# Optimization experiments

Measured on AMD Instinct MI355X. Metric: run time of the kernel, lower is better.

The kernel has to match this reference:

```python
import jax, jax.numpy as jnp
import numpy as np

N_NODES = 50000
N_EDGES = 800000
H = 64      # node_hidden_size
S = 16      # static_feature_size
EF = 16     # edge_feature_size
ATT_IN = 2 * H + 2 * S + EF   # 176
ATT_W = 2 * H + EF            # 144
UPD_IN = 2 * H                # 128
UPD_W = 2 * H                 # 128


def setup_inputs() -> dict:
    key = jax.random.key(0)
    ks = jax.random.split(key, 12)
    x = jax.random.normal(ks[0], (N_NODES, H), dtype=jnp.float32)
    x_s = jax.random.normal(ks[1], (N_NODES, S), dtype=jnp.float32)
    edge_index = jax.random.randint(ks[2], (2, N_EDGES), 0, N_NODES, dtype=jnp.int32)
    edge_features = jax.random.normal(ks[3], (N_EDGES, EF), dtype=jnp.float32)

    def lin(k, out_dim, in_dim):
        lim = 1.0 / np.sqrt(in_dim)
        kw, kb = jax.random.split(k)
        W = jax.random.uniform(kw, (out_dim, in_dim), minval=-lim, maxval=lim, dtype=jnp.float32)
        b = jax.random.uniform(kb, (out_dim,), minval=-lim, maxval=lim, dtype=jnp.float32)
        return W, b

    att_w1, att_b1 = lin(ks[4], ATT_W, ATT_IN)
    att_w2, att_b2 = lin(ks[5], 1, ATT_W)
    upd_w1, upd_b1 = lin(ks[6], UPD_W, UPD_IN)
    upd_w2, upd_b2 = lin(ks[7], H, UPD_W)

    return {
        "x": x, "x_s": x_s, "edge_index": edge_index, "edge_features": edge_features,
        "att_w1": att_w1, "att_b1": att_b1, "att_w2": att_w2, "att_b2": att_b2,
        "upd_w1": upd_w1, "upd_b1": upd_b1, "upd_w2": upd_w2, "upd_b2": upd_b2,
    }


def segment_softmax(scores, segment_ids, num_segments):
    max_scores = jax.ops.segment_max(scores, segment_ids, num_segments=num_segments)
    exp_scores = jnp.exp(scores - max_scores[segment_ids])
    sum_exp = jax.ops.segment_sum(exp_scores, segment_ids, num_segments=num_segments)
    return exp_scores / (sum_exp[segment_ids] + 1e-9)


def reference(x, x_s, edge_index, edge_features,
              att_w1, att_b1, att_w2, att_b2,
              upd_w1, upd_b1, upd_w2, upd_b2):
    num_nodes = x.shape[0]
    src, dst = edge_index[0], edge_index[1]

    # gather per-edge features: [E, 2H+2S+EF]
    att_in = jnp.concatenate(
        [x[src], x[dst], x_s[src], x_s[dst], edge_features], axis=-1)

    # attention MLP (depth=1, relu hidden), squeeze to [E]
    h = jax.nn.relu(att_in @ att_w1.T + att_b1)
    raw = (h @ att_w2.T + att_b2).squeeze(-1)
    raw = jax.nn.leaky_relu(raw)

    attn = segment_softmax(raw, dst, num_nodes)

    # weighted scatter-sum of source hidden feats -> [N, H]
    aggregated = jax.ops.segment_sum(x[src] * attn[:, None], dst, num_segments=num_nodes)

    upd_in = jnp.concatenate([x, aggregated], axis=-1)
    u = jax.nn.relu(upd_in @ upd_w1.T + upd_b1)
    out = u @ upd_w2.T + upd_b2
    return jax.nn.relu(out)
```

## Files before the change

### kernel.cpp

```cpp
#include <hip/hip_runtime.h>
#include <math.h>

#define N_NODES_C 50000
#define E_C       800000
#define ATT_IN_C  176
#define ATT_HID_C 144
#define SCAN_B    98
#define UPD_TILES 3125
#define DEG_B     3125
#define CVT_B     8228
#define SCORE_B   512
#define SCORE_WAVES (SCORE_B * 4)

typedef __attribute__((ext_vector_type(8))) __bf16 bf16x8;
typedef __attribute__((ext_vector_type(4))) float f32x4;

#define O_RAW   0L
#define O_DEG   3201024L
#define O_OFF   3402752L
#define O_CUR   3603456L
#define O_CSR   3804160L
#define O_EFB   16605184L
#define O_XB    42206208L
#define O_XSB   48607232L
#define O_W1B   50208256L
#define O_UW1B  50259968L
#define O_UW2B  50293760L
#define O_AGGB  50311168L
#define O_PSUM  O_AGGB

__device__ __forceinline__ bf16x8 bzero8() {
    bf16x8 z;
#pragma unroll
    for (int i = 0; i < 8; ++i) z[i] = (__bf16)0.0f;
    return z;
}

__global__ __launch_bounds__(256) void k_prep(
    const int* __restrict__ ei,
    const float* __restrict__ x, const float* __restrict__ xs,
    const float* __restrict__ ef, const float* __restrict__ w1,
    const float* __restrict__ uw1, const float* __restrict__ uw2,
    int* __restrict__ deg,
    __bf16* __restrict__ xb, __bf16* __restrict__ xsb,
    __bf16* __restrict__ efb, __bf16* __restrict__ w1b,
    __bf16* __restrict__ uw1b, __bf16* __restrict__ uw2b)
{
    int bid = blockIdx.x;
    if (bid < DEG_B) {
        int e = bid * 256 + threadIdx.x;
        if (e < E_C) atomicAdd(&deg[ei[E_C + e]], 1);
        return;
    }
    long g = (long)(bid - DEG_B) * 256 + threadIdx.x;
    const long G_X = 400000, G_XS = 500000, G_EF = 2100000,
               G_W1 = 2103168, G_UW1 = 2105216, G_UW2 = 2106240;
    if (g >= G_UW2) return;
    const float* src; __bf16* dst; long off;
    if (g < G_X)        { src = x;   dst = xb;   off = g * 8; }
    else if (g < G_XS)  { src = xs;  dst = xsb;  off = (g - G_X) * 8; }
    else if (g < G_EF)  { src = ef;  dst = efb;  off = (g - G_XS) * 8; }
    else if (g < G_W1)  { src = w1;  dst = w1b;  off = (g - G_EF) * 8; }
    else if (g < G_UW1) { src = uw1; dst = uw1b; off = (g - G_W1) * 8; }
    else                { src = uw2; dst = uw2b; off = (g - G_UW1) * 8; }
    float4 a = *(const float4*)(src + off);
    float4 b = *(const float4*)(src + off + 4);
    bf16x8 o;
    o[0] = (__bf16)a.x; o[1] = (__bf16)a.y; o[2] = (__bf16)a.z; o[3] = (__bf16)a.w;
    o[4] = (__bf16)b.x; o[5] = (__bf16)b.y; o[6] = (__bf16)b.z; o[7] = (__bf16)b.w;
    *(bf16x8*)(dst + off) = o;
}

__global__ __launch_bounds__(256) void k_scan1(const int* __restrict__ deg,
                                               int* __restrict__ psum) {
    __shared__ int red[256];
    int b = blockIdx.x, t = threadIdx.x;
    int i = b * 512 + t * 2;
    int s = 0;
    if (i < N_NODES_C) s += deg[i];
    if (i + 1 < N_NODES_C) s += deg[i + 1];
    red[t] = s;
    __syncthreads();
#pragma unroll
    for (int off = 128; off > 0; off >>= 1) {
        if (t < off) red[t] += red[t + off];
        __syncthreads();
    }
    if (t == 0) psum[b] = red[0];
}

__global__ __launch_bounds__(256) void k_scan3(const int* __restrict__ deg,
                                               const int* __restrict__ psum,
                                               int* __restrict__ offsets,
                                               int* __restrict__ cursor) {
    __shared__ int sc[256];
    __shared__ int bo[2];
    int b = blockIdx.x, t = threadIdx.x;
    if (t < 64) {
        int v1 = (t < SCAN_B) ? psum[t] : 0;
        int v2 = (t + 64 < SCAN_B) ? psum[t + 64] : 0;
        int c   = ((t < b) ? v1 : 0) + ((t + 64 < b) ? v2 : 0);
        int tot = v1 + v2;
#pragma unroll
        for (int off = 32; off > 0; off >>= 1) {
            c   += __shfl_xor(c, off, 64);
            tot += __shfl_xor(tot, off, 64);
        }
        if (t == 0) { bo[0] = c; bo[1] = tot; }
    }
    int i = b * 512 + t * 2;
    int d0 = (i < N_NODES_C) ? deg[i] : 0;
    int d1 = (i + 1 < N_NODES_C) ? deg[i + 1] : 0;
    int s = d0 + d1;
    sc[t] = s;
    __syncthreads();
#pragma unroll
    for (int off = 1; off < 256; off <<= 1) {
        int val = sc[t];
        int add = (t >= off) ? sc[t - off] : 0;
        __syncthreads();
        sc[t] = val + add;
        __syncthreads();
    }
    int excl = bo[0] + sc[t] - s;
    if (i < N_NODES_C)     { offsets[i]     = excl;      cursor[i]     = excl; }
    if (i + 1 < N_NODES_C) { offsets[i + 1] = excl + d0; cursor[i + 1] = excl + d0; }
    if (b == 0 && t == 0)  offsets[N_NODES_C] = bo[1];
}

__global__ __launch_bounds__(256) void k_fill(const int* __restrict__ ei,
                                              int* __restrict__ cursor,
                                              int4* __restrict__ csr) {
    int e = blockIdx.x * blockDim.x + threadIdx.x;
    if (e < E_C) {
        int src  = ei[e];
        int dst  = ei[E_C + e];
        int slot = atomicAdd(&cursor[dst], 1);
        csr[slot] = make_int4(src, dst, e, 0);
    }
}

__device__ __forceinline__ void load_afrags(
    int src, int dst, int e, int quad,
    const __bf16* __restrict__ xb, const __bf16* __restrict__ xsb,
    const __bf16* __restrict__ efb,
    bf16x8 a[6])
{
    const __bf16* px = xb + (long)src * 64 + quad * 8;
    const __bf16* pd = xb + (long)dst * 64 + quad * 8;
    a[0] = *(const bf16x8*)(px);
    a[1] = *(const bf16x8*)(px + 32);
    a[2] = *(const bf16x8*)(pd);
    a[3] = *(const bf16x8*)(pd + 32);
    if (quad < 2) {
        a[4] = *(const bf16x8*)(xsb + (long)src * 16 + quad * 8);
        a[5] = *(const bf16x8*)(efb + (long)e * 16 + quad * 8);
    } else {
        a[4] = *(const bf16x8*)(xsb + (long)dst * 16 + (quad - 2) * 8);
        a[5] = bzero8();
    }
}

__global__ __launch_bounds__(256) void k_scores_mfma(
    const __bf16* __restrict__ xb, const __bf16* __restrict__ xsb,
    const __bf16* __restrict__ efb, const __bf16* __restrict__ w1b,
    const int4* __restrict__ csr,
    const float* __restrict__ b1, const float* __restrict__ w2,
    const float* __restrict__ b2, float* __restrict__ raw)
{
    __shared__ __bf16 w1s[144 * 184];
    int tid  = threadIdx.x;
    int lane = tid & 63;

    for (int c = tid; c < 144 * 22; c += 256) {
        int n = c / 22, kk = (c % 22) * 8;
        *(bf16x8*)&w1s[n * 184 + kk] = *(const bf16x8*)(w1b + (long)n * ATT_IN_C + kk);
    }
    for (int n = tid; n < 144; n += 256)
        *(bf16x8*)&w1s[n * 184 + 176] = bzero8();
    __syncthreads();

    int w = blockIdx.x * 4 + (tid >> 6);
    const int NP = E_C / 32;
    int per = (NP + SCORE_WAVES - 1) / SCORE_WAVES;
    long j0 = (long)w * per;
    long j1 = j0 + per; if (j1 > NP) j1 = NP;
    if (j0 >= j1) return;

    int mrow = lane & 15;
    int quad = lane >> 4;
    const __bf16* wls = &w1s[mrow * 184 + quad * 8];

    float b1v[9], w2v[9];
#pragma unroll
    for (int nt = 0; nt < 9; ++nt) {
        int n = nt * 16 + mrow;
        b1v[nt] = b1[n];
        w2v[nt] = w2[n];
    }
    float b2v = b2[0];

    bf16x8 curA[6], curB[6], nxtA[6], nxtB[6];
    int4 cA = make_int4(0, 0, 0, 0), cB = cA;
    {
        int4 e0 = csr[j0 * 32 + mrow];
        int4 e1 = csr[j0 * 32 + 16 + mrow];
        load_afrags(e0.x, e0.y, e0.z, quad, xb, xsb, efb, curA);
        load_afrags(e1.x, e1.y, e1.z, quad, xb, xsb, efb, curB);
        if (j0 + 1 < j1) {
            int4 f0 = csr[(j0 + 1) * 32 + mrow];
            int4 f1 = csr[(j0 + 1) * 32 + 16 + mrow];
            load_afrags(f0.x, f0.y, f0.z, quad, xb, xsb, efb, nxtA);
            load_afrags(f1.x, f1.y, f1.z, quad, xb, xsb, efb, nxtB);
        }
    }

    for (long j = j0; j < j1; ++j) {
        if (j + 2 < j1) {
            cA = csr[(j + 2) * 32 + mrow];
            cB = csr[(j + 2) * 32 + 16 + mrow];
        }

        f32x4 accA[9], accB[9];
#pragma unroll
        for (int nt = 0; nt < 9; ++nt) {
            accA[nt] = (f32x4){0.f, 0.f, 0.f, 0.f};
            accB[nt] = (f32x4){0.f, 0.f, 0.f, 0.f};
        }

#pragma unroll
        for (int ks = 0; ks < 6; ++ks) {
#pragma unroll
            for (int nt = 0; nt < 9; ++nt) {
                bf16x8 bf = *(const bf16x8*)(wls + nt * (16 * 184) + ks * 32);
                accA[nt] = __builtin_amdgcn_mfma_f32_16x16x32_bf16(
                    curA[ks], bf, accA[nt], 0, 0, 0);
                accB[nt] = __builtin_amdgcn_mfma_f32_16x16x32_bf16(
                    curB[ks], bf, accB[nt], 0, 0, 0);
            }
        }

        float pA0 = 0.f, pA1 = 0.f, pA2 = 0.f, pA3 = 0.f;
        float pB0 = 0.f, pB1 = 0.f, pB2 = 0.f, pB3 = 0.f;
#pragma unroll
        for (int nt = 0; nt < 9; ++nt) {
            pA0 += w2v[nt] * fmaxf(accA[nt][0] + b1v[nt], 0.f);
            pA1 += w2v[nt] * fmaxf(accA[nt][1] + b1v[nt], 0.f);
            pA2 += w2v[nt] * fmaxf(accA[nt][2] + b1v[nt], 0.f);
            pA3 += w2v[nt] * fmaxf(accA[nt][3] + b1v[nt], 0.f);
            pB0 += w2v[nt] * fmaxf(accB[nt][0] + b1v[nt], 0.f);
            pB1 += w2v[nt] * fmaxf(accB[nt][1] + b1v[nt], 0.f);
            pB2 += w2v[nt] * fmaxf(accB[nt][2] + b1v[nt], 0.f);
            pB3 += w2v[nt] * fmaxf(accB[nt][3] + b1v[nt], 0.f);
        }
#pragma unroll
        for (int off = 1; off < 16; off <<= 1) {
            pA0 += __shfl_xor(pA0, off, 64);
            pA1 += __shfl_xor(pA1, off, 64);
            pA2 += __shfl_xor(pA2, off, 64);
            pA3 += __shfl_xor(pA3, off, 64);
            pB0 += __shfl_xor(pB0, off, 64);
            pB1 += __shfl_xor(pB1, off, 64);
            pB2 += __shfl_xor(pB2, off, 64);
            pB3 += __shfl_xor(pB3, off, 64);
        }
        if (mrow < 4) {
            float vA = (mrow == 0) ? pA0 : (mrow == 1) ? pA1 : (mrow == 2) ? pA2 : pA3;
            float vB = (mrow == 0) ? pB0 : (mrow == 1) ? pB1 : (mrow == 2) ? pB2 : pB3;
            vA += b2v; vB += b2v;
            vA = (vA >= 0.f) ? vA : 0.01f * vA;
            vB = (vB >= 0.f) ? vB : 0.01f * vB;
            raw[(j * 2) * 16 + quad * 4 + mrow]     = vA;
            raw[(j * 2 + 1) * 16 + quad * 4 + mrow] = vB;
        }

#pragma unroll
        for (int i = 0; i < 6; ++i) { curA[i] = nxtA[i]; curB[i] = nxtB[i]; }
        if (j + 2 < j1) {
            load_afrags(cA.x, cA.y, cA.z, quad, xb, xsb, efb, nxtA);
            load_afrags(cB.x, cB.y, cB.z, quad, xb, xsb, efb, nxtB);
        }
    }
}

__global__ __launch_bounds__(256) void k_agg(
    const __bf16* __restrict__ xb, const int* __restrict__ offsets,
    const int4* __restrict__ csr,
    const float* __restrict__ raw, __bf16* __restrict__ aggb)
{
    int tid = threadIdx.x;
    int wave = tid >> 6, lane = tid & 63;
    int v = blockIdx.x * 4 + wave;
    if (v >= N_NODES_C) return;
    int s0 = offsets[v], s1 = offsets[v + 1];

    float m = -INFINITY;
    for (int p = s0 + lane; p < s1; p += 64) m = fmaxf(m, raw[p]);
#pragma unroll
    for (int off = 32; off > 0; off >>= 1) m = fmaxf(m, __shfl_xor(m, off, 64));

    float acc = 0.f, sum = 0.f;
    int p = s0;
    for (; p + 4 <= s1; p += 4) {
        int4 c0 = csr[p], c1 = csr[p + 1], c2 = csr[p + 2], c3 = csr[p + 3];
        float r0 = raw[p], r1 = raw[p + 1], r2 = raw[p + 2], r3 = raw[p + 3];
        float v0 = (float)xb[(long)c0.x * 64 + lane];
        float v1 = (float)xb[(long)c1.x * 64 + lane];
        float v2 = (float)xb[(long)c2.x * 64 + lane];
        float v3 = (float)xb[(long)c3.x * 64 + lane];
        float w0 = expf(r0 - m), w1 = expf(r1 - m);
        float w2 = expf(r2 - m), w3 = expf(r3 - m);
        sum += (w0 + w1) + (w2 + w3);
        acc += w0 * v0 + w1 * v1 + w2 * v2 + w3 * v3;
    }
    for (; p < s1; ++p) {
        int src = csr[p].x;
        float w = expf(raw[p] - m);
        sum += w;
        acc += w * (float)xb[(long)src * 64 + lane];
    }
    aggb[(long)v * 64 + lane] = (__bf16)(acc / (sum + 1e-9f));
}

__global__ __launch_bounds__(256) void k_upd_mfma(
    const __bf16* __restrict__ xb, const __bf16* __restrict__ aggb,
    const __bf16* __restrict__ w1b, const float* __restrict__ b1,
    const __bf16* __restrict__ w2b, const float* __restrict__ b2,
    float* __restrict__ out)
{
    __shared__ __bf16 ubuf[4][16 * 136];
    int tid = threadIdx.x, wid = tid >> 6, lane = tid & 63;
    int tile = blockIdx.x * 4 + wid;
    if (tile >= UPD_TILES) return;
    int mrow = lane & 15, quad = lane >> 4;

    long node = (long)tile * 16 + mrow;
    bf16x8 a1[4];
    a1[0] = *(const bf16x8*)(xb + node * 64 + quad * 8);
    a1[1] = *(const bf16x8*)(xb + node * 64 + 32 + quad * 8);
    a1[2] = *(const bf16x8*)(aggb + node * 64 + quad * 8);
    a1[3] = *(const bf16x8*)(aggb + node * 64 + 32 + quad * 8);

    bf16x8 b1f[4][8];
#pragma unroll
    for (int ks = 0; ks < 4; ++ks)
#pragma unroll
        for (int nt = 0; nt < 8; ++nt)
            b1f[ks][nt] = *(const bf16x8*)(w1b + (long)(nt * 16 + mrow) * 128 + ks * 32 + quad * 8);

    f32x4 acc1[8];
#pragma unroll
    for (int nt = 0; nt < 8; ++nt) acc1[nt] = (f32x4){0.f, 0.f, 0.f, 0.f};
#pragma unroll
    for (int ks = 0; ks < 4; ++ks)
#pragma unroll
        for (int nt = 0; nt < 8; ++nt)
            acc1[nt] = __builtin_amdgcn_mfma_f32_16x16x32_bf16(a1[ks], b1f[ks][nt], acc1[nt], 0, 0, 0);

    __bf16* ub = ubuf[wid];
#pragma unroll
    for (int nt = 0; nt < 8; ++nt) {
        float bb = b1[nt * 16 + mrow];
#pragma unroll
        for (int r = 0; r < 4; ++r) {
            float h = fmaxf(acc1[nt][r] + bb, 0.f);
            ub[(quad * 4 + r) * 136 + nt * 16 + mrow] = (__bf16)h;
        }
    }

    bf16x8 a2[4];
#pragma unroll
    for (int ks = 0; ks < 4; ++ks)
        a2[ks] = *(bf16x8*)&ub[mrow * 136 + ks * 32 + quad * 8];

    bf16x8 b2f[4][4];
#pragma unroll
    for (int ks = 0; ks < 4; ++ks)
#pragma unroll
        for (int nt = 0; nt < 4; ++nt)
            b2f[ks][nt] = *(const bf16x8*)(w2b + (long)(nt * 16 + mrow) * 128 + ks * 32 + quad * 8);

    f32x4 acc2[4];
#pragma unroll
    for (int nt = 0; nt < 4; ++nt) acc2[nt] = (f32x4){0.f, 0.f, 0.f, 0.f};
#pragma unroll
    for (int ks = 0; ks < 4; ++ks)
#pragma unroll
        for (int nt = 0; nt < 4; ++nt)
            acc2[nt] = __builtin_amdgcn_mfma_f32_16x16x32_bf16(a2[ks], b2f[ks][nt], acc2[nt], 0, 0, 0);

#pragma unroll
    for (int nt = 0; nt < 4; ++nt) {
        float bb = b2[nt * 16 + mrow];
#pragma unroll
        for (int r = 0; r < 4; ++r) {
            long nodeo = (long)tile * 16 + quad * 4 + r;
            out[nodeo * 64 + nt * 16 + mrow] = fmaxf(acc2[nt][r] + bb, 0.f);
        }
    }
}

extern "C" void kernel_launch(void* const* d_in, const int* in_sizes, int n_in,
                              void* d_out, int out_size, void* d_ws, size_t ws_size,
                              hipStream_t stream) {
    const float* x    = (const float*)d_in[0];
    const float* xs   = (const float*)d_in[1];
    const int*   ei   = (const int*)d_in[2];
    const float* ef   = (const float*)d_in[3];
    const float* aw1  = (const float*)d_in[4];
    const float* ab1  = (const float*)d_in[5];
    const float* aw2  = (const float*)d_in[6];
    const float* ab2  = (const float*)d_in[7];
    const float* uw1  = (const float*)d_in[8];
    const float* ub1  = (const float*)d_in[9];
    const float* uw2  = (const float*)d_in[10];
    const float* ub2  = (const float*)d_in[11];
    float* out = (float*)d_out;

    char* ws = (char*)d_ws;
    float*  raw     = (float*)(ws + O_RAW);
    int*    deg     = (int*)(ws + O_DEG);
    int*    offsets = (int*)(ws + O_OFF);
    int*    cursor  = (int*)(ws + O_CUR);
    int4*   csr     = (int4*)(ws + O_CSR);
    __bf16* efb     = (__bf16*)(ws + O_EFB);
    __bf16* xb      = (__bf16*)(ws + O_XB);
    __bf16* xsb     = (__bf16*)(ws + O_XSB);
    __bf16* w1b     = (__bf16*)(ws + O_W1B);
    __bf16* uw1b    = (__bf16*)(ws + O_UW1B);
    __bf16* uw2b    = (__bf16*)(ws + O_UW2B);
    __bf16* aggb    = (__bf16*)(ws + O_AGGB);
    int*    psum    = (int*)(ws + O_PSUM);

    hipMemsetAsync(deg, 0, N_NODES_C * sizeof(int), stream);
    hipLaunchKernelGGL(k_prep,     dim3(DEG_B + CVT_B),           dim3(256), 0, stream,
                       ei, x, xs, ef, aw1, uw1, uw2, deg, xb, xsb, efb, w1b, uw1b, uw2b);
    hipLaunchKernelGGL(k_scan1,    dim3(SCAN_B),                  dim3(256), 0, stream, deg, psum);
    hipLaunchKernelGGL(k_scan3,    dim3(SCAN_B),                  dim3(256), 0, stream,
                       deg, psum, offsets, cursor);
    hipLaunchKernelGGL(k_fill,     dim3((E_C + 255) / 256),       dim3(256), 0, stream,
                       ei, cursor, csr);
    hipLaunchKernelGGL(k_scores_mfma, dim3(SCORE_B),              dim3(256), 0, stream,
                       xb, xsb, efb, w1b, csr, ab1, aw2, ab2, raw);
    hipLaunchKernelGGL(k_agg,      dim3((N_NODES_C + 3) / 4),     dim3(256), 0, stream,
                       xb, offsets, csr, raw, aggb);
    hipLaunchKernelGGL(k_upd_mfma, dim3((UPD_TILES + 3) / 4),     dim3(256), 0, stream,
                       xb, aggb, uw1b, ub1, uw2b, ub2, out);
}
```

Before: 374.0 us.

## Precompute per-node destination projection and pack CSR entries into 32 bits

Splits the attention first-layer matmul so the destination-node terms (x[dst], x_s[dst]) plus bias are computed once per node in a new kernel and stored as fp16. The per-edge MFMA loop then covers only source and edge features, halving its K depth, and gathers the precomputed destination partials. CSR entries are packed as 16-bit src and dst in one word, and edge features are converted to bf16 in CSR order inside the fill kernel. The packing assumes node ids fit in 16 bits, but N_NODES is 50000 and fits. The fp16 partial sums and the extra gathers add some rounding error and memory traffic.

```diff
diff --git a/kernel.cpp b/kernel.cpp
--- a/kernel.cpp
+++ b/kernel.cpp
@@ -8,26 +8,29 @@
 #define SCAN_B    98
 #define UPD_TILES 3125
 #define DEG_B     3125
-#define CVT_B     8228
+#define CVT_B     1978
 #define SCORE_B   512
 #define SCORE_WAVES (SCORE_B * 4)
 
 typedef __attribute__((ext_vector_type(8))) __bf16 bf16x8;
+typedef __attribute__((ext_vector_type(8))) _Float16 h16x8;
 typedef __attribute__((ext_vector_type(4))) float f32x4;
 
 #define O_RAW   0L
-#define O_DEG   3201024L
-#define O_OFF   3402752L
-#define O_CUR   3603456L
-#define O_CSR   3804160L
-#define O_EFB   16605184L
-#define O_XB    42206208L
-#define O_XSB   48607232L
-#define O_W1B   50208256L
-#define O_UW1B  50259968L
-#define O_UW2B  50293760L
-#define O_AGGB  50311168L
-#define O_PSUM  O_AGGB
+#define O_DEG   3200000L
+#define O_OFF   3400704L
+#define O_CUR   3601408L
+#define O_CSR   3802112L
+#define O_EFC   7002112L
+#define O_XB    32602112L
+#define O_XSB   39002112L
+#define O_W1B   40602112L
+#define O_UW1B  40653312L
+#define O_UW2B  40686080L
+#define O_P8    40702464L
+#define O_P1    53502464L
+#define O_PSUM  O_P8
+#define O_AGGB  O_P8
 
 __device__ __forceinline__ bf16x8 bzero8() {
     bf16x8 z;
@@ -39,11 +42,11 @@
 __global__ __launch_bounds__(256) void k_prep(
     const int* __restrict__ ei,
     const float* __restrict__ x, const float* __restrict__ xs,
-    const float* __restrict__ ef, const float* __restrict__ w1,
+    const float* __restrict__ w1,
     const float* __restrict__ uw1, const float* __restrict__ uw2,
     int* __restrict__ deg,
     __bf16* __restrict__ xb, __bf16* __restrict__ xsb,
-    __bf16* __restrict__ efb, __bf16* __restrict__ w1b,
+    __bf16* __restrict__ w1b,
     __bf16* __restrict__ uw1b, __bf16* __restrict__ uw2b)
 {
     int bid = blockIdx.x;
@@ -53,14 +56,13 @@
         return;
     }
     long g = (long)(bid - DEG_B) * 256 + threadIdx.x;
-    const long G_X = 400000, G_XS = 500000, G_EF = 2100000,
-               G_W1 = 2103168, G_UW1 = 2105216, G_UW2 = 2106240;
+    const long G_X = 400000, G_XS = 500000, G_W1 = 503168,
+               G_UW1 = 505216, G_UW2 = 506240;
     if (g >= G_UW2) return;
     const float* src; __bf16* dst; long off;
     if (g < G_X)        { src = x;   dst = xb;   off = g * 8; }
     else if (g < G_XS)  { src = xs;  dst = xsb;  off = (g - G_X) * 8; }
-    else if (g < G_EF)  { src = ef;  dst = efb;  off = (g - G_XS) * 8; }
-    else if (g < G_W1)  { src = w1;  dst = w1b;  off = (g - G_EF) * 8; }
+    else if (g < G_W1)  { src = w1;  dst = w1b;  off = (g - G_XS) * 8; }
     else if (g < G_UW1) { src = uw1; dst = uw1b; off = (g - G_W1) * 8; }
     else                { src = uw2; dst = uw2b; off = (g - G_UW1) * 8; }
     float4 a = *(const float4*)(src + off);
@@ -129,55 +131,115 @@
 }
 
 __global__ __launch_bounds__(256) void k_fill(const int* __restrict__ ei,
+                                              const float* __restrict__ ef,
                                               int* __restrict__ cursor,
-                                              int4* __restrict__ csr) {
+                                              unsigned* __restrict__ csrp,
+                                              __bf16* __restrict__ efc) {
     int e = blockIdx.x * blockDim.x + threadIdx.x;
     if (e < E_C) {
         int src  = ei[e];
         int dst  = ei[E_C + e];
         int slot = atomicAdd(&cursor[dst], 1);
-        csr[slot] = make_int4(src, dst, e, 0);
-    }
-}
-
-__device__ __forceinline__ void load_afrags(
-    int src, int dst, int e, int quad,
+        csrp[slot] = (unsigned)src | ((unsigned)dst << 16);
+        const float4* efp = (const float4*)(ef + (long)e * 16);
+        float4 f0 = efp[0], f1 = efp[1], f2 = efp[2], f3 = efp[3];
+        bf16x8 o0, o1;
+        o0[0] = (__bf16)f0.x; o0[1] = (__bf16)f0.y; o0[2] = (__bf16)f0.z; o0[3] = (__bf16)f0.w;
+        o0[4] = (__bf16)f1.x; o0[5] = (__bf16)f1.y; o0[6] = (__bf16)f1.z; o0[7] = (__bf16)f1.w;
+        o1[0] = (__bf16)f2.x; o1[1] = (__bf16)f2.y; o1[2] = (__bf16)f2.z; o1[3] = (__bf16)f2.w;
+        o1[4] = (__bf16)f3.x; o1[5] = (__bf16)f3.y; o1[6] = (__bf16)f3.z; o1[7] = (__bf16)f3.w;
+        __bf16* d = efc + (long)slot * 16;
+        *(bf16x8*)d       = o0;
+        *(bf16x8*)(d + 8) = o1;
+    }
+}
+
+__global__ __launch_bounds__(256) void k_nodep(
     const __bf16* __restrict__ xb, const __bf16* __restrict__ xsb,
-    const __bf16* __restrict__ efb,
-    bf16x8 a[6])
+    const __bf16* __restrict__ w1b, const float* __restrict__ b1,
+    _Float16* __restrict__ p8, _Float16* __restrict__ p1)
+{
+    __shared__ _Float16 tbuf[4][16 * 256];
+    int tid = threadIdx.x, wid = tid >> 6, lane = tid & 63;
+    int tile = blockIdx.x * 4 + wid;
+    if (tile >= UPD_TILES) return;
+    int mrow = lane & 15, quad = lane >> 4;
+
+    long node = (long)tile * 16 + mrow;
+    bf16x8 a0 = *(const bf16x8*)(xb + node * 64 + quad * 8);
+    bf16x8 a1 = *(const bf16x8*)(xb + node * 64 + 32 + quad * 8);
+    bf16x8 a2 = (quad < 2) ? *(const bf16x8*)(xsb + node * 16 + quad * 8) : bzero8();
+
+    f32x4 acc[9];
+#pragma unroll
+    for (int nt = 0; nt < 9; ++nt) acc[nt] = (f32x4){0.f, 0.f, 0.f, 0.f};
+#pragma unroll
+    for (int nt = 0; nt < 9; ++nt) {
+        long n = nt * 16 + mrow;
+        bf16x8 b0 = *(const bf16x8*)(w1b + n * 176 + 64 + quad * 8);
+        bf16x8 bm = *(const bf16x8*)(w1b + n * 176 + 96 + quad * 8);
+        bf16x8 b2 = (quad < 2) ? *(const bf16x8*)(w1b + n * 176 + 144 + quad * 8)
+                               : bzero8();
+        acc[nt] = __builtin_amdgcn_mfma_f32_16x16x32_bf16(a0, b0, acc[nt], 0, 0, 0);
+        acc[nt] = __builtin_amdgcn_mfma_f32_16x16x32_bf16(a1, bm, acc[nt], 0, 0, 0);
+        acc[nt] = __builtin_amdgcn_mfma_f32_16x16x32_bf16(a2, b2, acc[nt], 0, 0, 0);
+    }
+
+    _Float16* tb = tbuf[wid];
+#pragma unroll
+    for (int nt = 0; nt < 9; ++nt) {
+        float bb = b1[nt * 16 + mrow];
+#pragma unroll
+        for (int r = 0; r < 4; ++r)
+            tb[(quad * 4 + r) * 256 + mrow * 16 + nt] = (_Float16)(acc[nt][r] + bb);
+    }
+    long g8 = (long)tile * 2048;
+#pragma unroll
+    for (int c = 0; c < 4; ++c) {
+        int idx = c * 64 + lane;
+        int nl = idx >> 4, mr = idx & 15;
+        *(h16x8*)(p8 + g8 + (long)idx * 8) = *(const h16x8*)(tb + nl * 256 + mr * 16);
+    }
+    long g1 = (long)tile * 256;
+#pragma unroll
+    for (int c = 0; c < 4; ++c) {
+        int idx = lane * 4 + c;
+        int nl = idx >> 4, mr = idx & 15;
+        p1[g1 + idx] = tb[nl * 256 + mr * 16 + 8];
+    }
+}
+
+__device__ __forceinline__ void load_afrags2(
+    int src, long slot, int quad,
+    const __bf16* __restrict__ xb, const __bf16* __restrict__ xsb,
+    const __bf16* __restrict__ efc,
+    bf16x8 a[3])
 {
     const __bf16* px = xb + (long)src * 64 + quad * 8;
-    const __bf16* pd = xb + (long)dst * 64 + quad * 8;
     a[0] = *(const bf16x8*)(px);
     a[1] = *(const bf16x8*)(px + 32);
-    a[2] = *(const bf16x8*)(pd);
-    a[3] = *(const bf16x8*)(pd + 32);
-    if (quad < 2) {
-        a[4] = *(const bf16x8*)(xsb + (long)src * 16 + quad * 8);
-        a[5] = *(const bf16x8*)(efb + (long)e * 16 + quad * 8);
-    } else {
-        a[4] = *(const bf16x8*)(xsb + (long)dst * 16 + (quad - 2) * 8);
-        a[5] = bzero8();
-    }
-}
-
-__global__ __launch_bounds__(256) void k_scores_mfma(
+    a[2] = (quad < 2) ? *(const bf16x8*)(xsb + (long)src * 16 + quad * 8)
+                      : *(const bf16x8*)(efc + slot * 16 + (quad - 2) * 8);
+}
+
+__global__ __launch_bounds__(256, 2) void k_scores_mfma(
     const __bf16* __restrict__ xb, const __bf16* __restrict__ xsb,
-    const __bf16* __restrict__ efb, const __bf16* __restrict__ w1b,
-    const int4* __restrict__ csr,
-    const float* __restrict__ b1, const float* __restrict__ w2,
-    const float* __restrict__ b2, float* __restrict__ raw)
+    const __bf16* __restrict__ efc, const __bf16* __restrict__ w1b,
+    const unsigned* __restrict__ csrp,
+    const _Float16* __restrict__ p8, const _Float16* __restrict__ p1,
+    const float* __restrict__ w2, const float* __restrict__ b2,
+    float* __restrict__ raw)
 {
-    __shared__ __bf16 w1s[144 * 184];
+    __shared__ __bf16 w1s[144 * 104];
     int tid  = threadIdx.x;
     int lane = tid & 63;
 
-    for (int c = tid; c < 144 * 22; c += 256) {
-        int n = c / 22, kk = (c % 22) * 8;
-        *(bf16x8*)&w1s[n * 184 + kk] = *(const bf16x8*)(w1b + (long)n * ATT_IN_C + kk);
-    }
-    for (int n = tid; n < 144; n += 256)
-        *(bf16x8*)&w1s[n * 184 + 176] = bzero8();
+    for (int c = tid; c < 144 * 12; c += 256) {
+        int n = c / 12, kk = c % 12;
+        int col = (kk < 8) ? kk * 8 : (kk < 10) ? 128 + (kk - 8) * 8
+                                                : 160 + (kk - 10) * 8;
+        *(bf16x8*)&w1s[n * 104 + kk * 8] = *(const bf16x8*)(w1b + (long)n * ATT_IN_C + col);
+    }
     __syncthreads();
 
     int w = blockIdx.x * 4 + (tid >> 6);
@@ -189,36 +251,35 @@
 
     int mrow = lane & 15;
     int quad = lane >> 4;
-    const __bf16* wls = &w1s[mrow * 184 + quad * 8];
-
-    float b1v[9], w2v[9];
-#pragma unroll
-    for (int nt = 0; nt < 9; ++nt) {
-        int n = nt * 16 + mrow;
-        b1v[nt] = b1[n];
-        w2v[nt] = w2[n];
-    }
+    const __bf16* wls = &w1s[mrow * 104 + quad * 8];
+
+    float w2v[9];
+#pragma unroll
+    for (int nt = 0; nt < 9; ++nt) w2v[nt] = w2[nt * 16 + mrow];
     float b2v = b2[0];
 
-    bf16x8 curA[6], curB[6], nxtA[6], nxtB[6];
-    int4 cA = make_int4(0, 0, 0, 0), cB = cA;
+    bf16x8 curA[3], curB[3], nxtA[3], nxtB[3];
+    int curDA = 0, curDB = 0, nxtDA = 0, nxtDB = 0;
+    unsigned cA = 0, cB = 0;
     {
-        int4 e0 = csr[j0 * 32 + mrow];
-        int4 e1 = csr[j0 * 32 + 16 + mrow];
-        load_afrags(e0.x, e0.y, e0.z, quad, xb, xsb, efb, curA);
-        load_afrags(e1.x, e1.y, e1.z, quad, xb, xsb, efb, curB);
+        unsigned e0 = csrp[j0 * 32 + mrow];
+        unsigned e1 = csrp[j0 * 32 + 16 + mrow];
+        curDA = (int)(e0 >> 16); curDB = (int)(e1 >> 16);
+        load_afrags2((int)(e0 & 0xFFFFu), j0 * 32 + mrow,      quad, xb, xsb, efc, curA);
+        load_afrags2((int)(e1 & 0xFFFFu), j0 * 32 + 16 + mrow, quad, xb, xsb, efc, curB);
         if (j0 + 1 < j1) {
-            int4 f0 = csr[(j0 + 1) * 32 + mrow];
-            int4 f1 = csr[(j0 + 1) * 32 + 16 + mrow];
-            load_afrags(f0.x, f0.y, f0.z, quad, xb, xsb, efb, nxtA);
-            load_afrags(f1.x, f1.y, f1.z, quad, xb, xsb, efb, nxtB);
+            unsigned f0 = csrp[(j0 + 1) * 32 + mrow];
+            unsigned f1 = csrp[(j0 + 1) * 32 + 16 + mrow];
+            nxtDA = (int)(f0 >> 16); nxtDB = (int)(f1 >> 16);
+            load_afrags2((int)(f0 & 0xFFFFu), (j0 + 1) * 32 + mrow,      quad, xb, xsb, efc, nxtA);
+            load_afrags2((int)(f1 & 0xFFFFu), (j0 + 1) * 32 + 16 + mrow, quad, xb, xsb, efc, nxtB);
         }
     }
 
     for (long j = j0; j < j1; ++j) {
         if (j + 2 < j1) {
-            cA = csr[(j + 2) * 32 + mrow];
-            cB = csr[(j + 2) * 32 + 16 + mrow];
+            cA = csrp[(j + 2) * 32 + mrow];
+            cB = csrp[(j + 2) * 32 + 16 + mrow];
         }
 
         f32x4 accA[9], accB[9];
@@ -229,10 +290,10 @@
         }
 
 #pragma unroll
-        for (int ks = 0; ks < 6; ++ks) {
+        for (int ks = 0; ks < 3; ++ks) {
 #pragma unroll
             for (int nt = 0; nt < 9; ++nt) {
-                bf16x8 bf = *(const bf16x8*)(wls + nt * (16 * 184) + ks * 32);
+                bf16x8 bf = *(const bf16x8*)(wls + nt * (16 * 104) + ks * 32);
                 accA[nt] = __builtin_amdgcn_mfma_f32_16x16x32_bf16(
                     curA[ks], bf, accA[nt], 0, 0, 0);
                 accB[nt] = __builtin_amdgcn_mfma_f32_16x16x32_bf16(
@@ -240,19 +301,45 @@
             }
         }
 
+        int dA[4], dB[4];
+#pragma unroll
+        for (int r = 0; r < 4; ++r) {
+            int sl = (lane & 48) | (quad * 4 + r);
+            dA[r] = __shfl(curDA, sl, 64);
+            dB[r] = __shfl(curDB, sl, 64);
+        }
+        h16x8 paf[4], pbf[4];
+        float pa8[4], pb8[4];
+#pragma unroll
+        for (int r = 0; r < 4; ++r) {
+            paf[r] = *(const h16x8*)(p8 + (long)dA[r] * 128 + mrow * 8);
+            pa8[r] = (float)p1[(long)dA[r] * 16 + mrow];
+            pbf[r] = *(const h16x8*)(p8 + (long)dB[r] * 128 + mrow * 8);
+            pb8[r] = (float)p1[(long)dB[r] * 16 + mrow];
+        }
+
         float pA0 = 0.f, pA1 = 0.f, pA2 = 0.f, pA3 = 0.f;
         float pB0 = 0.f, pB1 = 0.f, pB2 = 0.f, pB3 = 0.f;
 #pragma unroll
-        for (int nt = 0; nt < 9; ++nt) {
-            pA0 += w2v[nt] * fmaxf(accA[nt][0] + b1v[nt], 0.f);
-            pA1 += w2v[nt] * fmaxf(accA[nt][1] + b1v[nt], 0.f);
-            pA2 += w2v[nt] * fmaxf(accA[nt][2] + b1v[nt], 0.f);
-            pA3 += w2v[nt] * fmaxf(accA[nt][3] + b1v[nt], 0.f);
-            pB0 += w2v[nt] * fmaxf(accB[nt][0] + b1v[nt], 0.f);
-            pB1 += w2v[nt] * fmaxf(accB[nt][1] + b1v[nt], 0.f);
-            pB2 += w2v[nt] * fmaxf(accB[nt][2] + b1v[nt], 0.f);
-            pB3 += w2v[nt] * fmaxf(accB[nt][3] + b1v[nt], 0.f);
-        }
+        for (int nt = 0; nt < 8; ++nt) {
+            pA0 += w2v[nt] * fmaxf(accA[nt][0] + (float)paf[0][nt], 0.f);
+            pA1 += w2v[nt] * fmaxf(accA[nt][1] + (float)paf[1][nt], 0.f);
+            pA2 += w2v[nt] * fmaxf(accA[nt][2] + (float)paf[2][nt], 0.f);
+            pA3 += w2v[nt] * fmaxf(accA[nt][3] + (float)paf[3][nt], 0.f);
+            pB0 += w2v[nt] * fmaxf(accB[nt][0] + (float)pbf[0][nt], 0.f);
+            pB1 += w2v[nt] * fmaxf(accB[nt][1] + (float)pbf[1][nt], 0.f);
+            pB2 += w2v[nt] * fmaxf(accB[nt][2] + (float)pbf[2][nt], 0.f);
+            pB3 += w2v[nt] * fmaxf(accB[nt][3] + (float)pbf[3][nt], 0.f);
+        }
+        pA0 += w2v[8] * fmaxf(accA[8][0] + pa8[0], 0.f);
+        pA1 += w2v[8] * fmaxf(accA[8][1] + pa8[1], 0.f);
+        pA2 += w2v[8] * fmaxf(accA[8][2] + pa8[2], 0.f);
+        pA3 += w2v[8] * fmaxf(accA[8][3] + pa8[3], 0.f);
+        pB0 += w2v[8] * fmaxf(accB[8][0] + pb8[0], 0.f);
+        pB1 += w2v[8] * fmaxf(accB[8][1] + pb8[1], 0.f);
+        pB2 += w2v[8] * fmaxf(accB[8][2] + pb8[2], 0.f);
+        pB3 += w2v[8] * fmaxf(accB[8][3] + pb8[3], 0.f);
+
 #pragma unroll
         for (int off = 1; off < 16; off <<= 1) {
             pA0 += __shfl_xor(pA0, off, 64);
@@ -275,17 +362,19 @@
         }
 
 #pragma unroll
-        for (int i = 0; i < 6; ++i) { curA[i] = nxtA[i]; curB[i] = nxtB[i]; }
+        for (int i = 0; i < 3; ++i) { curA[i] = nxtA[i]; curB[i] = nxtB[i]; }
+        curDA = nxtDA; curDB = nxtDB;
         if (j + 2 < j1) {
-            load_afrags(cA.x, cA.y, cA.z, quad, xb, xsb, efb, nxtA);
-            load_afrags(cB.x, cB.y, cB.z, quad, xb, xsb, efb, nxtB);
+            nxtDA = (int)(cA >> 16); nxtDB = (int)(cB >> 16);
+            load_afrags2((int)(cA & 0xFFFFu), (j + 2) * 32 + mrow,      quad, xb, xsb, efc, nxtA);
+            load_afrags2((int)(cB & 0xFFFFu), (j + 2) * 32 + 16 + mrow, quad, xb, xsb, efc, nxtB);
         }
     }
 }
 
 __global__ __launch_bounds__(256) void k_agg(
     const __bf16* __restrict__ xb, const int* __restrict__ offsets,
-    const int4* __restrict__ csr,
+    const unsigned* __restrict__ csrp,
     const float* __restrict__ raw, __bf16* __restrict__ aggb)
 {
     int tid = threadIdx.x;
@@ -302,19 +391,19 @@
     float acc = 0.f, sum = 0.f;
     int p = s0;
     for (; p + 4 <= s1; p += 4) {
-        int4 c0 = csr[p], c1 = csr[p + 1], c2 = csr[p + 2], c3 = csr[p + 3];
+        unsigned c0 = csrp[p], c1 = csrp[p + 1], c2 = csrp[p + 2], c3 = csrp[p + 3];
         float r0 = raw[p], r1 = raw[p + 1], r2 = raw[p + 2], r3 = raw[p + 3];
-        float v0 = (float)xb[(long)c0.x * 64 + lane];
-        float v1 = (float)xb[(long)c1.x * 64 + lane];
-        float v2 = (float)xb[(long)c2.x * 64 + lane];
-        float v3 = (float)xb[(long)c3.x * 64 + lane];
+        float v0 = (float)xb[(long)(c0 & 0xFFFFu) * 64 + lane];
+        float v1 = (float)xb[(long)(c1 & 0xFFFFu) * 64 + lane];
+        float v2 = (float)xb[(long)(c2 & 0xFFFFu) * 64 + lane];
+        float v3 = (float)xb[(long)(c3 & 0xFFFFu) * 64 + lane];
         float w0 = expf(r0 - m), w1 = expf(r1 - m);
         float w2 = expf(r2 - m), w3 = expf(r3 - m);
         sum += (w0 + w1) + (w2 + w3);
         acc += w0 * v0 + w1 * v1 + w2 * v2 + w3 * v3;
     }
     for (; p < s1; ++p) {
-        int src = csr[p].x;
+        int src = (int)(csrp[p] & 0xFFFFu);
         float w = expf(raw[p] - m);
         sum += w;
         acc += w * (float)xb[(long)src * 64 + lane];
@@ -418,32 +507,36 @@
     float* out = (float*)d_out;
 
     char* ws = (char*)d_ws;
-    float*  raw     = (float*)(ws + O_RAW);
-    int*    deg     = (int*)(ws + O_DEG);
-    int*    offsets = (int*)(ws + O_OFF);
-    int*    cursor  = (int*)(ws + O_CUR);
-    int4*   csr     = (int4*)(ws + O_CSR);
-    __bf16* efb     = (__bf16*)(ws + O_EFB);
-    __bf16* xb      = (__bf16*)(ws + O_XB);
-    __bf16* xsb     = (__bf16*)(ws + O_XSB);
-    __bf16* w1b     = (__bf16*)(ws + O_W1B);
-    __bf16* uw1b    = (__bf16*)(ws + O_UW1B);
-    __bf16* uw2b    = (__bf16*)(ws + O_UW2B);
-    __bf16* aggb    = (__bf16*)(ws + O_AGGB);
-    int*    psum    = (int*)(ws + O_PSUM);
+    float*     raw     = (float*)(ws + O_RAW);
+    int*       deg     = (int*)(ws + O_DEG);
+    int*       offsets = (int*)(ws + O_OFF);
+    int*       cursor  = (int*)(ws + O_CUR);
+    unsigned*  csrp    = (unsigned*)(ws + O_CSR);
+    __bf16*    efc     = (__bf16*)(ws + O_EFC);
+    __bf16*    xb      = (__bf16*)(ws + O_XB);
+    __bf16*    xsb     = (__bf16*)(ws + O_XSB);
+    __bf16*    w1b     = (__bf16*)(ws + O_W1B);
+    __bf16*    uw1b    = (__bf16*)(ws + O_UW1B);
+    __bf16*    uw2b    = (__bf16*)(ws + O_UW2B);
+    _Float16*  p8      = (_Float16*)(ws + O_P8);
+    _Float16*  p1      = (_Float16*)(ws + O_P1);
+    __bf16*    aggb    = (__bf16*)(ws + O_AGGB);
+    int*       psum    = (int*)(ws + O_PSUM);
 
     hipMemsetAsync(deg, 0, N_NODES_C * sizeof(int), stream);
     hipLaunchKernelGGL(k_prep,     dim3(DEG_B + CVT_B),           dim3(256), 0, stream,
-                       ei, x, xs, ef, aw1, uw1, uw2, deg, xb, xsb, efb, w1b, uw1b, uw2b);
+                       ei, x, xs, aw1, uw1, uw2, deg, xb, xsb, w1b, uw1b, uw2b);
     hipLaunchKernelGGL(k_scan1,    dim3(SCAN_B),                  dim3(256), 0, stream, deg, psum);
     hipLaunchKernelGGL(k_scan3,    dim3(SCAN_B),                  dim3(256), 0, stream,
                        deg, psum, offsets, cursor);
     hipLaunchKernelGGL(k_fill,     dim3((E_C + 255) / 256),       dim3(256), 0, stream,
-                       ei, cursor, csr);
+                       ei, ef, cursor, csrp, efc);
+    hipLaunchKernelGGL(k_nodep,    dim3((UPD_TILES + 3) / 4),     dim3(256), 0, stream,
+                       xb, xsb, w1b, ab1, p8, p1);
     hipLaunchKernelGGL(k_scores_mfma, dim3(SCORE_B),              dim3(256), 0, stream,
-                       xb, xsb, efb, w1b, csr, ab1, aw2, ab2, raw);
+                       xb, xsb, efc, w1b, csrp, p8, p1, aw2, ab2, raw);
     hipLaunchKernelGGL(k_agg,      dim3((N_NODES_C + 3) / 4),     dim3(256), 0, stream,
-                       xb, offsets, csr, raw, aggb);
+                       xb, offsets, csrp, raw, aggb);
     hipLaunchKernelGGL(k_upd_mfma, dim3((UPD_TILES + 3) / 4),     dim3(256), 0, stream,
                        xb, aggb, uw1b, ub1, uw2b, ub2, out);
 }
```

Result: slower. 408.1 us (+9.1%).

## Pack CSR into 16-bit src/dst words and permute edge features during fill

Applied to the files above, without the earlier changes.

Replaces the 16-byte int4 CSR records with one 32-bit word holding 16-bit src and dst. It also moves the edge-feature bf16 conversion into the fill kernel, writing the features in CSR slot order so the score kernel reads them contiguously instead of gathering by edge id. The score kernel now processes one 16-edge tile per iteration instead of two, with a deeper index prefetch, more blocks and a launch-bounds occupancy hint. This cuts CSR and edge-feature traffic, but the 16-bit packing only works because node ids stay below 65536.

```diff
diff --git a/kernel.cpp b/kernel.cpp
--- a/kernel.cpp
+++ b/kernel.cpp
@@ -8,25 +8,25 @@
 #define SCAN_B    98
 #define UPD_TILES 3125
 #define DEG_B     3125
-#define CVT_B     8228
-#define SCORE_B   512
+#define CVT_B     1978
+#define SCORE_B   768
 #define SCORE_WAVES (SCORE_B * 4)
 
 typedef __attribute__((ext_vector_type(8))) __bf16 bf16x8;
 typedef __attribute__((ext_vector_type(4))) float f32x4;
 
 #define O_RAW   0L
-#define O_DEG   3201024L
-#define O_OFF   3402752L
-#define O_CUR   3603456L
-#define O_CSR   3804160L
-#define O_EFB   16605184L
-#define O_XB    42206208L
-#define O_XSB   48607232L
-#define O_W1B   50208256L
-#define O_UW1B  50259968L
-#define O_UW2B  50293760L
-#define O_AGGB  50311168L
+#define O_DEG   3200000L
+#define O_OFF   3400704L
+#define O_CUR   3601408L
+#define O_CSR   3802112L
+#define O_EFC   7002112L
+#define O_XB    32602112L
+#define O_XSB   39002112L
+#define O_W1B   40602112L
+#define O_UW1B  40653312L
+#define O_UW2B  40686080L
+#define O_AGGB  40702464L
 #define O_PSUM  O_AGGB
 
 __device__ __forceinline__ bf16x8 bzero8() {
@@ -39,11 +39,11 @@
 __global__ __launch_bounds__(256) void k_prep(
     const int* __restrict__ ei,
     const float* __restrict__ x, const float* __restrict__ xs,
-    const float* __restrict__ ef, const float* __restrict__ w1,
+    const float* __restrict__ w1,
     const float* __restrict__ uw1, const float* __restrict__ uw2,
     int* __restrict__ deg,
     __bf16* __restrict__ xb, __bf16* __restrict__ xsb,
-    __bf16* __restrict__ efb, __bf16* __restrict__ w1b,
+    __bf16* __restrict__ w1b,
     __bf16* __restrict__ uw1b, __bf16* __restrict__ uw2b)
 {
     int bid = blockIdx.x;
@@ -53,14 +53,13 @@
         return;
     }
     long g = (long)(bid - DEG_B) * 256 + threadIdx.x;
-    const long G_X = 400000, G_XS = 500000, G_EF = 2100000,
-               G_W1 = 2103168, G_UW1 = 2105216, G_UW2 = 2106240;
+    const long G_X = 400000, G_XS = 500000, G_W1 = 503168,
+               G_UW1 = 505216, G_UW2 = 506240;
     if (g >= G_UW2) return;
     const float* src; __bf16* dst; long off;
     if (g < G_X)        { src = x;   dst = xb;   off = g * 8; }
     else if (g < G_XS)  { src = xs;  dst = xsb;  off = (g - G_X) * 8; }
-    else if (g < G_EF)  { src = ef;  dst = efb;  off = (g - G_XS) * 8; }
-    else if (g < G_W1)  { src = w1;  dst = w1b;  off = (g - G_EF) * 8; }
+    else if (g < G_W1)  { src = w1;  dst = w1b;  off = (g - G_XS) * 8; }
     else if (g < G_UW1) { src = uw1; dst = uw1b; off = (g - G_W1) * 8; }
     else                { src = uw2; dst = uw2b; off = (g - G_UW1) * 8; }
     float4 a = *(const float4*)(src + off);
@@ -129,21 +128,33 @@
 }
 
 __global__ __launch_bounds__(256) void k_fill(const int* __restrict__ ei,
+                                              const float* __restrict__ ef,
                                               int* __restrict__ cursor,
-                                              int4* __restrict__ csr) {
+                                              unsigned* __restrict__ csrp,
+                                              __bf16* __restrict__ efc) {
     int e = blockIdx.x * blockDim.x + threadIdx.x;
     if (e < E_C) {
         int src  = ei[e];
         int dst  = ei[E_C + e];
         int slot = atomicAdd(&cursor[dst], 1);
-        csr[slot] = make_int4(src, dst, e, 0);
+        csrp[slot] = (unsigned)src | ((unsigned)dst << 16);
+        const float4* efp = (const float4*)(ef + (long)e * 16);
+        float4 f0 = efp[0], f1 = efp[1], f2 = efp[2], f3 = efp[3];
+        bf16x8 o0, o1;
+        o0[0] = (__bf16)f0.x; o0[1] = (__bf16)f0.y; o0[2] = (__bf16)f0.z; o0[3] = (__bf16)f0.w;
+        o0[4] = (__bf16)f1.x; o0[5] = (__bf16)f1.y; o0[6] = (__bf16)f1.z; o0[7] = (__bf16)f1.w;
+        o1[0] = (__bf16)f2.x; o1[1] = (__bf16)f2.y; o1[2] = (__bf16)f2.z; o1[3] = (__bf16)f2.w;
+        o1[4] = (__bf16)f3.x; o1[5] = (__bf16)f3.y; o1[6] = (__bf16)f3.z; o1[7] = (__bf16)f3.w;
+        __bf16* d = efc + (long)slot * 16;
+        *(bf16x8*)d       = o0;
+        *(bf16x8*)(d + 8) = o1;
     }
 }
 
 __device__ __forceinline__ void load_afrags(
-    int src, int dst, int e, int quad,
+    int src, int dst, long slot, int quad,
     const __bf16* __restrict__ xb, const __bf16* __restrict__ xsb,
-    const __bf16* __restrict__ efb,
+    const __bf16* __restrict__ efc,
     bf16x8 a[6])
 {
     const __bf16* px = xb + (long)src * 64 + quad * 8;
@@ -154,17 +165,17 @@
     a[3] = *(const bf16x8*)(pd + 32);
     if (quad < 2) {
         a[4] = *(const bf16x8*)(xsb + (long)src * 16 + quad * 8);
-        a[5] = *(const bf16x8*)(efb + (long)e * 16 + quad * 8);
+        a[5] = *(const bf16x8*)(efc + slot * 16 + quad * 8);
     } else {
         a[4] = *(const bf16x8*)(xsb + (long)dst * 16 + (quad - 2) * 8);
         a[5] = bzero8();
     }
 }
 
-__global__ __launch_bounds__(256) void k_scores_mfma(
+__global__ __launch_bounds__(256, 3) void k_scores_mfma(
     const __bf16* __restrict__ xb, const __bf16* __restrict__ xsb,
-    const __bf16* __restrict__ efb, const __bf16* __restrict__ w1b,
-    const int4* __restrict__ csr,
+    const __bf16* __restrict__ efc, const __bf16* __restrict__ w1b,
+    const unsigned* __restrict__ csrp,
     const float* __restrict__ b1, const float* __restrict__ w2,
     const float* __restrict__ b2, float* __restrict__ raw)
 {
@@ -181,10 +192,10 @@
     __syncthreads();
 
     int w = blockIdx.x * 4 + (tid >> 6);
-    const int NP = E_C / 32;
-    int per = (NP + SCORE_WAVES - 1) / SCORE_WAVES;
+    const int NT = E_C / 16;
+    int per = (NT + SCORE_WAVES - 1) / SCORE_WAVES;
     long j0 = (long)w * per;
-    long j1 = j0 + per; if (j1 > NP) j1 = NP;
+    long j1 = j0 + per; if (j1 > NT) j1 = NT;
     if (j0 >= j1) return;
 
     int mrow = lane & 15;
@@ -200,92 +211,72 @@
     }
     float b2v = b2[0];
 
-    bf16x8 curA[6], curB[6], nxtA[6], nxtB[6];
-    int4 cA = make_int4(0, 0, 0, 0), cB = cA;
+    bf16x8 cur[6], nxt[6];
+    unsigned creg = 0, cnext = 0;
     {
-        int4 e0 = csr[j0 * 32 + mrow];
-        int4 e1 = csr[j0 * 32 + 16 + mrow];
-        load_afrags(e0.x, e0.y, e0.z, quad, xb, xsb, efb, curA);
-        load_afrags(e1.x, e1.y, e1.z, quad, xb, xsb, efb, curB);
+        unsigned e0 = csrp[j0 * 16 + mrow];
+        load_afrags((int)(e0 & 0xFFFFu), (int)(e0 >> 16), j0 * 16 + mrow,
+                    quad, xb, xsb, efc, cur);
         if (j0 + 1 < j1) {
-            int4 f0 = csr[(j0 + 1) * 32 + mrow];
-            int4 f1 = csr[(j0 + 1) * 32 + 16 + mrow];
-            load_afrags(f0.x, f0.y, f0.z, quad, xb, xsb, efb, nxtA);
-            load_afrags(f1.x, f1.y, f1.z, quad, xb, xsb, efb, nxtB);
-        }
+            unsigned e1 = csrp[(j0 + 1) * 16 + mrow];
+            load_afrags((int)(e1 & 0xFFFFu), (int)(e1 >> 16), (j0 + 1) * 16 + mrow,
+                        quad, xb, xsb, efc, nxt);
+        }
+        if (j0 + 2 < j1) creg = csrp[(j0 + 2) * 16 + mrow];
     }
 
     for (long j = j0; j < j1; ++j) {
-        if (j + 2 < j1) {
-            cA = csr[(j + 2) * 32 + mrow];
-            cB = csr[(j + 2) * 32 + 16 + mrow];
-        }
-
-        f32x4 accA[9], accB[9];
-#pragma unroll
-        for (int nt = 0; nt < 9; ++nt) {
-            accA[nt] = (f32x4){0.f, 0.f, 0.f, 0.f};
-            accB[nt] = (f32x4){0.f, 0.f, 0.f, 0.f};
-        }
+        if (j + 3 < j1) cnext = csrp[(j + 3) * 16 + mrow];
+
+        f32x4 acc[9];
+#pragma unroll
+        for (int nt = 0; nt < 9; ++nt) acc[nt] = (f32x4){0.f, 0.f, 0.f, 0.f};
 
 #pragma unroll
         for (int ks = 0; ks < 6; ++ks) {
 #pragma unroll
             for (int nt = 0; nt < 9; ++nt) {
                 bf16x8 bf = *(const bf16x8*)(wls + nt * (16 * 184) + ks * 32);
-                accA[nt] = __builtin_amdgcn_mfma_f32_16x16x32_bf16(
-                    curA[ks], bf, accA[nt], 0, 0, 0);
-                accB[nt] = __builtin_amdgcn_mfma_f32_16x16x32_bf16(
-                    curB[ks], bf, accB[nt], 0, 0, 0);
+                acc[nt] = __builtin_amdgcn_mfma_f32_16x16x32_bf16(
+                    cur[ks], bf, acc[nt], 0, 0, 0);
             }
         }
 
-        float pA0 = 0.f, pA1 = 0.f, pA2 = 0.f, pA3 = 0.f;
-        float pB0 = 0.f, pB1 = 0.f, pB2 = 0.f, pB3 = 0.f;
+        float p0 = 0.f, p1 = 0.f, p2 = 0.f, p3 = 0.f;
 #pragma unroll
         for (int nt = 0; nt < 9; ++nt) {
-            pA0 += w2v[nt] * fmaxf(accA[nt][0] + b1v[nt], 0.f);
-            pA1 += w2v[nt] * fmaxf(accA[nt][1] + b1v[nt], 0.f);
-            pA2 += w2v[nt] * fmaxf(accA[nt][2] + b1v[nt], 0.f);
-            pA3 += w2v[nt] * fmaxf(accA[nt][3] + b1v[nt], 0.f);
-            pB0 += w2v[nt] * fmaxf(accB[nt][0] + b1v[nt], 0.f);
-            pB1 += w2v[nt] * fmaxf(accB[nt][1] + b1v[nt], 0.f);
-            pB2 += w2v[nt] * fmaxf(accB[nt][2] + b1v[nt], 0.f);
-            pB3 += w2v[nt] * fmaxf(accB[nt][3] + b1v[nt], 0.f);
+            p0 += w2v[nt] * fmaxf(acc[nt][0] + b1v[nt], 0.f);
+            p1 += w2v[nt] * fmaxf(acc[nt][1] + b1v[nt], 0.f);
+            p2 += w2v[nt] * fmaxf(acc[nt][2] + b1v[nt], 0.f);
+            p3 += w2v[nt] * fmaxf(acc[nt][3] + b1v[nt], 0.f);
         }
 #pragma unroll
         for (int off = 1; off < 16; off <<= 1) {
-            pA0 += __shfl_xor(pA0, off, 64);
-            pA1 += __shfl_xor(pA1, off, 64);
-            pA2 += __shfl_xor(pA2, off, 64);
-            pA3 += __shfl_xor(pA3, off, 64);
-            pB0 += __shfl_xor(pB0, off, 64);
-            pB1 += __shfl_xor(pB1, off, 64);
-            pB2 += __shfl_xor(pB2, off, 64);
-            pB3 += __shfl_xor(pB3, off, 64);
+            p0 += __shfl_xor(p0, off, 64);
+            p1 += __shfl_xor(p1, off, 64);
+            p2 += __shfl_xor(p2, off, 64);
+            p3 += __shfl_xor(p3, off, 64);
         }
         if (mrow < 4) {
-            float vA = (mrow == 0) ? pA0 : (mrow == 1) ? pA1 : (mrow == 2) ? pA2 : pA3;
-            float vB = (mrow == 0) ? pB0 : (mrow == 1) ? pB1 : (mrow == 2) ? pB2 : pB3;
-            vA += b2v; vB += b2v;
-            vA = (vA >= 0.f) ? vA : 0.01f * vA;
-            vB = (vB >= 0.f) ? vB : 0.01f * vB;
-            raw[(j * 2) * 16 + quad * 4 + mrow]     = vA;
-            raw[(j * 2 + 1) * 16 + quad * 4 + mrow] = vB;
-        }
-
-#pragma unroll
-        for (int i = 0; i < 6; ++i) { curA[i] = nxtA[i]; curB[i] = nxtB[i]; }
+            float v = (mrow == 0) ? p0 : (mrow == 1) ? p1 : (mrow == 2) ? p2 : p3;
+            v += b2v;
+            v = (v >= 0.f) ? v : 0.01f * v;
+            raw[j * 16 + quad * 4 + mrow] = v;
+        }
+
+#pragma unroll
+        for (int i = 0; i < 6; ++i) cur[i] = nxt[i];
         if (j + 2 < j1) {
-            load_afrags(cA.x, cA.y, cA.z, quad, xb, xsb, efb, nxtA);
-            load_afrags(cB.x, cB.y, cB.z, quad, xb, xsb, efb, nxtB);
-        }
+            load_afrags((int)(creg & 0xFFFFu), (int)(creg >> 16), (j + 2) * 16 + mrow,
+                        quad, xb, xsb, efc, nxt);
+        }
+        creg = cnext;
     }
 }
 
 __global__ __launch_bounds__(256) void k_agg(
     const __bf16* __restrict__ xb, const int* __restrict__ offsets,
-    const int4* __restrict__ csr,
+    const unsigned* __restrict__ csrp,
     const float* __restrict__ raw, __bf16* __restrict__ aggb)
 {
     int tid = threadIdx.x;
@@ -302,19 +293,19 @@
     float acc = 0.f, sum = 0.f;
     int p = s0;
     for (; p + 4 <= s1; p += 4) {
-        int4 c0 = csr[p], c1 = csr[p + 1], c2 = csr[p + 2], c3 = csr[p + 3];
+        unsigned c0 = csrp[p], c1 = csrp[p + 1], c2 = csrp[p + 2], c3 = csrp[p + 3];
         float r0 = raw[p], r1 = raw[p + 1], r2 = raw[p + 2], r3 = raw[p + 3];
-        float v0 = (float)xb[(long)c0.x * 64 + lane];
-        float v1 = (float)xb[(long)c1.x * 64 + lane];
-        float v2 = (float)xb[(long)c2.x * 64 + lane];
-        float v3 = (float)xb[(long)c3.x * 64 + lane];
+        float v0 = (float)xb[(long)(c0 & 0xFFFFu) * 64 + lane];
+        float v1 = (float)xb[(long)(c1 & 0xFFFFu) * 64 + lane];
+        float v2 = (float)xb[(long)(c2 & 0xFFFFu) * 64 + lane];
+        float v3 = (float)xb[(long)(c3 & 0xFFFFu) * 64 + lane];
         float w0 = expf(r0 - m), w1 = expf(r1 - m);
         float w2 = expf(r2 - m), w3 = expf(r3 - m);
         sum += (w0 + w1) + (w2 + w3);
         acc += w0 * v0 + w1 * v1 + w2 * v2 + w3 * v3;
     }
     for (; p < s1; ++p) {
-        int src = csr[p].x;
+        int src = (int)(csrp[p] & 0xFFFFu);
         float w = expf(raw[p] - m);
         sum += w;
         acc += w * (float)xb[(long)src * 64 + lane];
@@ -418,32 +409,32 @@
     float* out = (float*)d_out;
 
     char* ws = (char*)d_ws;
-    float*  raw     = (float*)(ws + O_RAW);
-    int*    deg     = (int*)(ws + O_DEG);
-    int*    offsets = (int*)(ws + O_OFF);
-    int*    cursor  = (int*)(ws + O_CUR);
-    int4*   csr     = (int4*)(ws + O_CSR);
-    __bf16* efb     = (__bf16*)(ws + O_EFB);
-    __bf16* xb      = (__bf16*)(ws + O_XB);
-    __bf16* xsb     = (__bf16*)(ws + O_XSB);
-    __bf16* w1b     = (__bf16*)(ws + O_W1B);
-    __bf16* uw1b    = (__bf16*)(ws + O_UW1B);
-    __bf16* uw2b    = (__bf16*)(ws + O_UW2B);
-    __bf16* aggb    = (__bf16*)(ws + O_AGGB);
-    int*    psum    = (int*)(ws + O_PSUM);
+    float*     raw     = (float*)(ws + O_RAW);
+    int*       deg     = (int*)(ws + O_DEG);
+    int*       offsets = (int*)(ws + O_OFF);
+    int*       cursor  = (int*)(ws + O_CUR);
+    unsigned*  csrp    = (unsigned*)(ws + O_CSR);
+    __bf16*    efc     = (__bf16*)(ws + O_EFC);
+    __bf16*    xb      = (__bf16*)(ws + O_XB);
+    __bf16*    xsb     = (__bf16*)(ws + O_XSB);
+    __bf16*    w1b     = (__bf16*)(ws + O_W1B);
+    __bf16*    uw1b    = (__bf16*)(ws + O_UW1B);
+    __bf16*    uw2b    = (__bf16*)(ws + O_UW2B);
+    __bf16*    aggb    = (__bf16*)(ws + O_AGGB);
+    int*       psum    = (int*)(ws + O_PSUM);
 
     hipMemsetAsync(deg, 0, N_NODES_C * sizeof(int), stream);
     hipLaunchKernelGGL(k_prep,     dim3(DEG_B + CVT_B),           dim3(256), 0, stream,
-                       ei, x, xs, ef, aw1, uw1, uw2, deg, xb, xsb, efb, w1b, uw1b, uw2b);
+                       ei, x, xs, aw1, uw1, uw2, deg, xb, xsb, w1b, uw1b, uw2b);
     hipLaunchKernelGGL(k_scan1,    dim3(SCAN_B),                  dim3(256), 0, stream, deg, psum);
     hipLaunchKernelGGL(k_scan3,    dim3(SCAN_B),                  dim3(256), 0, stream,
                        deg, psum, offsets, cursor);
     hipLaunchKernelGGL(k_fill,     dim3((E_C + 255) / 256),       dim3(256), 0, stream,
-                       ei, cursor, csr);
+                       ei, ef, cursor, csrp, efc);
     hipLaunchKernelGGL(k_scores_mfma, dim3(SCORE_B),              dim3(256), 0, stream,
-                       xb, xsb, efb, w1b, csr, ab1, aw2, ab2, raw);
+                       xb, xsb, efc, w1b, csrp, ab1, aw2, ab2, raw);
     hipLaunchKernelGGL(k_agg,      dim3((N_NODES_C + 3) / 4),     dim3(256), 0, stream,
-                       xb, offsets, csr, raw, aggb);
+                       xb, offsets, csrp, raw, aggb);
     hipLaunchKernelGGL(k_upd_mfma, dim3((UPD_TILES + 3) / 4),     dim3(256), 0, stream,
                        xb, aggb, uw1b, ub1, uw2b, ub2, out);
 }
```

Result: slower. 621.3 us (+66.1%).
